# Kernel tuning notes

Measured on AMD Instinct MI355X. Metric: run time of the kernel, lower is better.

## Reference

```python
import jax, jax.numpy as jnp
import numpy as np

N_LAYERS = 2
N_QUBITS = 2


def _ry(t):
    c, s = jnp.cos(t / 2), jnp.sin(t / 2)
    m = jnp.stack([jnp.stack([c, -s], -1), jnp.stack([s, c], -1)], -2)
    return m.astype(jnp.complex64)


def _rx(t):
    c = jnp.cos(t / 2).astype(jnp.complex64)
    s = (-1j) * jnp.sin(t / 2).astype(jnp.complex64)
    return jnp.stack([jnp.stack([c, s], -1), jnp.stack([s, c], -1)], -2)


def _rz(t):
    e = jnp.exp(-0.5j * t.astype(jnp.complex64))
    z = jnp.zeros_like(e)
    return jnp.stack([jnp.stack([e, z], -1), jnp.stack([z, jnp.conj(e)], -1)], -2)


def _apply_w0(G, s):
    # gate on wire 0 (most significant); s: [N,2,2] indexed [n, q0, q1]
    if G.ndim == 2:
        G = G[None]
    return jnp.matmul(G, s)


def _apply_w1(G, s):
    # gate on wire 1: contract last index with G
    if G.ndim == 2:
        G = G[None]
    return jnp.matmul(s, jnp.swapaxes(G, -1, -2))


def _qnn_batched(enc, qw):
    # enc: [N,2] float angles; qw: [2,2,3] trainable angles.
    # Batched 2-qubit statevector simulation, state shape [N,2,2] (q0,q1).
    N = enc.shape[0]
    s = jnp.zeros((N, 2, 2), jnp.complex64).at[:, 0, 0].set(1.0)
    # data encoding: RY(enc_i) on wire i
    s = _apply_w0(_ry(enc[:, 0]), s)
    s = _apply_w1(_ry(enc[:, 1]), s)
    for l in range(N_LAYERS):
        # RX then RY then RZ on each qubit => fused single-qubit gate RZ@RY@RX
        g0 = _rz(qw[l, 0, 2]) @ _ry(qw[l, 0, 1]) @ _rx(qw[l, 0, 0])
        g1 = _rz(qw[l, 1, 2]) @ _ry(qw[l, 1, 1]) @ _rx(qw[l, 1, 0])
        s = _apply_w0(g0, s)
        s = _apply_w1(g1, s)
        # CNOT(control=0, target=1): flip q1 where q0 == 1
        s = s.at[:, 1, :].set(s[:, 1, ::-1])
    p = (s * jnp.conj(s)).real  # probabilities [N,2,2]
    z0 = (p[:, 0, :] - p[:, 1, :]).sum(-1)
    z1 = (p[:, :, 0] - p[:, :, 1]).sum(-1)
    return jnp.stack([z0, z1], -1)  # [N,2]


def _mlp(x, w1, b1, w2, b2, w3, b3):
    h = jnp.tanh(x @ w1 + b1)
    h = jnp.tanh(h @ w2 + b2)
    return h @ w3 + b3


def setup_inputs() -> dict:
    key = jax.random.key(0)
    ks = jax.random.split(key, 15)
    N = 1_000_000
    W = 32

    def rn(k, shape, scale):
        return (scale * jax.random.normal(k, shape)).astype(jnp.float32)

    return {
        "x": rn(ks[0], (N, 1), 1.0),
        "pre_w1": rn(ks[1], (1, W), 1.0),
        "pre_b1": rn(ks[2], (W,), 0.1),
        "pre_w2": rn(ks[3], (W, W), 1.0 / np.sqrt(W)),
        "pre_b2": rn(ks[4], (W,), 0.1),
        "pre_w3": rn(ks[5], (W, 2), 1.0 / np.sqrt(W)),
        "pre_b3": rn(ks[6], (2,), 0.1),
        "q_weights": rn(ks[7], (N_LAYERS, N_QUBITS, 3), 0.1),
        "post_w1": rn(ks[8], (2, W), 1.0 / np.sqrt(2)),
        "post_b1": rn(ks[9], (W,), 0.1),
        "post_w2": rn(ks[10], (W, W), 1.0 / np.sqrt(W)),
        "post_b2": rn(ks[11], (W,), 0.1),
        "post_w3": rn(ks[12], (W, 1), 1.0 / np.sqrt(W)),
        "post_b3": rn(ks[13], (1,), 0.1),
    }


def reference(x, pre_w1, pre_b1, pre_w2, pre_b2, pre_w3, pre_b3, q_weights,
              post_w1, post_b1, post_w2, post_b2, post_w3, post_b3):
    q = _mlp(x, pre_w1, pre_b1, pre_w2, pre_b2, pre_w3, pre_b3)        # [N,2]
    qhat = _qnn_batched(q, q_weights)                                  # [N,2]
    u = _mlp(qhat, post_w1, post_b1, post_w2, post_b2, post_w3, post_b3)  # [N,1]
    return u
```

## Files before the change

### kernel.cpp

```cpp
#include <hip/hip_runtime.h>
#include <math.h>
#include <stdint.h>


typedef __attribute__((ext_vector_type(8))) short short8;
typedef __attribute__((ext_vector_type(4))) float f32x4;

union Frag { uint32_t u[4]; short8 s; };

__device__ __forceinline__ float fast_tanh(float x) {
    float e = __expf(2.0f * x);
    return fmaf(-2.0f, __builtin_amdgcn_rcpf(e + 1.0f), 1.0f);
}

__device__ __forceinline__ void split8(const float h[8], uint32_t hi[4], uint32_t lo[4]) {
    #pragma unroll
    for (int p = 0; p < 4; ++p) {
        uint32_t u0 = __float_as_uint(h[2*p])   & 0xFFFF0000u;
        uint32_t u1 = __float_as_uint(h[2*p+1]) & 0xFFFF0000u;
        float l0 = h[2*p]   - __uint_as_float(u0);
        float l1 = h[2*p+1] - __uint_as_float(u1);
        uint32_t v0 = __float_as_uint(l0) & 0xFFFF0000u;
        uint32_t v1 = __float_as_uint(l1) & 0xFFFF0000u;
        hi[p] = (u0 >> 16) | u1;
        lo[p] = (v0 >> 16) | v1;
    }
}

struct cplx { float re, im; };
__device__ __forceinline__ cplx cmul(cplx a, cplx b) {
    return { a.re * b.re - a.im * b.im, a.re * b.im + a.im * b.re };
}
__device__ __forceinline__ cplx cadd(cplx a, cplx b) {
    return { a.re + b.re, a.im + b.im };
}

__global__ void qcpinn_setup(const float* __restrict__ qw,
                             const float* __restrict__ pw2,
                             const float* __restrict__ ow2,
                             float* __restrict__ ws) {
    const int lane = threadIdx.x & 63;
    const int s = lane & 15, gg = lane >> 4;
    uint32_t* wsu = (uint32_t*)ws;

    #pragma unroll
    for (int m = 0; m < 2; ++m) {
        const float* W = m ? ow2 : pw2;
        #pragma unroll
        for (int r = 0; r < 2; ++r) {
            float v[8];
            #pragma unroll
            for (int j = 0; j < 8; ++j)
                v[j] = W[(gg * 8 + j) * 32 + (r * 16 + s)];
            uint32_t hi[4], lo[4];
            split8(v, hi, lo);
            int bh = 32 + ((m * 4 + r * 2 + 0) * 64 + lane) * 4;
            int bl = 32 + ((m * 4 + r * 2 + 1) * 64 + lane) * 4;
            #pragma unroll
            for (int p = 0; p < 4; ++p) { wsu[bh + p] = hi[p]; wsu[bl + p] = lo[p]; }
        }
    }

    if (threadIdx.x == 0) {
        cplx U[16];
        for (int i = 0; i < 16; ++i) U[i] = {0.f, 0.f};
        U[0].re = U[5].re = U[10].re = U[15].re = 1.f;

        for (int l = 0; l < 2; ++l) {
            cplx g[2][4];
            for (int w = 0; w < 2; ++w) {
                float a = qw[l * 6 + w * 3 + 0];
                float b = qw[l * 6 + w * 3 + 1];
                float c = qw[l * 6 + w * 3 + 2];
                float sa, ca, sb, cb, sc, cc;
                __sincosf(0.5f * a, &sa, &ca);
                __sincosf(0.5f * b, &sb, &cb);
                __sincosf(0.5f * c, &sc, &cc);
                cplx RX[4] = {{ca, 0.f}, {0.f, -sa}, {0.f, -sa}, {ca, 0.f}};
                cplx RY[4] = {{cb, 0.f}, {-sb, 0.f}, {sb, 0.f}, {cb, 0.f}};
                cplx RZ[4] = {{cc, -sc}, {0.f, 0.f}, {0.f, 0.f}, {cc, sc}};
                cplx T[4];
                for (int i2 = 0; i2 < 2; ++i2)
                    for (int j2 = 0; j2 < 2; ++j2) {
                        cplx acc = {0.f, 0.f};
                        for (int k2 = 0; k2 < 2; ++k2)
                            acc = cadd(acc, cmul(RY[i2 * 2 + k2], RX[k2 * 2 + j2]));
                        T[i2 * 2 + j2] = acc;
                    }
                for (int i2 = 0; i2 < 2; ++i2)
                    for (int j2 = 0; j2 < 2; ++j2) {
                        cplx acc = {0.f, 0.f};
                        for (int k2 = 0; k2 < 2; ++k2)
                            acc = cadd(acc, cmul(RZ[i2 * 2 + k2], T[k2 * 2 + j2]));
                        g[w][i2 * 2 + j2] = acc;
                    }
            }
            cplx L[16];
            for (int i4 = 0; i4 < 4; ++i4) {
                int si = (i4 == 2) ? 3 : (i4 == 3) ? 2 : i4;
                for (int j4 = 0; j4 < 4; ++j4)
                    L[i4 * 4 + j4] = cmul(g[1][(si & 1) * 2 + (j4 & 1)],
                                          g[0][(si >> 1) * 2 + (j4 >> 1)]);
            }
            cplx Un[16];
            for (int i4 = 0; i4 < 4; ++i4)
                for (int j4 = 0; j4 < 4; ++j4) {
                    cplx acc = {0.f, 0.f};
                    for (int k4 = 0; k4 < 4; ++k4)
                        acc = cadd(acc, cmul(L[i4 * 4 + k4], U[k4 * 4 + j4]));
                    Un[i4 * 4 + j4] = acc;
                }
            for (int i = 0; i < 16; ++i) U[i] = Un[i];
        }
        for (int i = 0; i < 16; ++i) { ws[i] = U[i].re; ws[16 + i] = U[i].im; }
    }
}

__global__ __launch_bounds__(128) void qcpinn_main(
    const float* __restrict__ x,
    const float* __restrict__ pw1, const float* __restrict__ pb1,
    const float* __restrict__ pb2, const float* __restrict__ pw3,
    const float* __restrict__ pb3,
    const float* __restrict__ ws,
    const float* __restrict__ ow1, const float* __restrict__ ob1,
    const float* __restrict__ ob2, const float* __restrict__ ow3,
    const float* __restrict__ ob3,
    float* __restrict__ out, int N)
{
    const int lane = threadIdx.x & 63;
    const int wid  = threadIdx.x >> 6;
    const int s    = lane & 15;
    const int g    = lane >> 4;
    const int wave_id = blockIdx.x * 2 + wid;

    int samp[2];
    samp[0] = wave_id * 32 + s;
    samp[1] = samp[0] + 16;

    const float* U = ws;
    const Frag* fragp = (const Frag*)(ws + 32);

    float xv[2];
    xv[0] = (samp[0] < N) ? x[samp[0]] : 0.f;
    xv[1] = (samp[1] < N) ? x[samp[1]] : 0.f;

    f32x4 w1a = *(const f32x4*)(pw1 + g * 8);
    f32x4 w1b = *(const f32x4*)(pw1 + g * 8 + 4);
    f32x4 b1a = *(const f32x4*)(pb1 + g * 8);
    f32x4 b1b = *(const f32x4*)(pb1 + g * 8 + 4);

    Frag Bh[2], Bl[2];
    #pragma unroll
    for (int t = 0; t < 2; ++t) {
        float h[8];
        #pragma unroll
        for (int j = 0; j < 4; ++j) {
            h[j]     = fast_tanh(fmaf(xv[t], w1a[j], b1a[j]));
            h[4 + j] = fast_tanh(fmaf(xv[t], w1b[j], b1b[j]));
        }
        split8(h, Bh[t].u, Bl[t].u);
    }

    Frag A0h = fragp[0 * 64 + lane];
    Frag A0l = fragp[1 * 64 + lane];
    Frag A1h = fragp[2 * 64 + lane];
    Frag A1l = fragp[3 * 64 + lane];

    f32x4 pb2a = *(const f32x4*)(pb2 + g * 4);
    f32x4 pb2b = *(const f32x4*)(pb2 + 16 + g * 4);

    float h2[2][8];
    #pragma unroll
    for (int t = 0; t < 2; ++t) {
        f32x4 C0 = {0.f, 0.f, 0.f, 0.f};
        f32x4 C1 = {0.f, 0.f, 0.f, 0.f};
        C0 = __builtin_amdgcn_mfma_f32_16x16x32_bf16(A0h.s, Bh[t].s, C0, 0, 0, 0);
        C0 = __builtin_amdgcn_mfma_f32_16x16x32_bf16(A0h.s, Bl[t].s, C0, 0, 0, 0);
        C0 = __builtin_amdgcn_mfma_f32_16x16x32_bf16(A0l.s, Bh[t].s, C0, 0, 0, 0);
        C1 = __builtin_amdgcn_mfma_f32_16x16x32_bf16(A1h.s, Bh[t].s, C1, 0, 0, 0);
        C1 = __builtin_amdgcn_mfma_f32_16x16x32_bf16(A1h.s, Bl[t].s, C1, 0, 0, 0);
        C1 = __builtin_amdgcn_mfma_f32_16x16x32_bf16(A1l.s, Bh[t].s, C1, 0, 0, 0);
        #pragma unroll
        for (int i = 0; i < 4; ++i) {
            h2[t][i]     = fast_tanh(C0[i] + pb2a[i]);
            h2[t][4 + i] = fast_tanh(C1[i] + pb2b[i]);
        }
    }

    f32x4 w3a = *(const f32x4*)(pw3 + g * 8);
    f32x4 w3b = *(const f32x4*)(pw3 + g * 8 + 4);
    f32x4 w3c = *(const f32x4*)(pw3 + 32 + g * 8);
    f32x4 w3d = *(const f32x4*)(pw3 + 32 + g * 8 + 4);
    float bq0 = pb3[0], bq1 = pb3[1];

    float z0[2], z1[2];
    #pragma unroll
    for (int t = 0; t < 2; ++t) {
        float q0 = 0.f, q1 = 0.f;
        q0 = fmaf(h2[t][0], w3a[0], q0); q1 = fmaf(h2[t][0], w3a[1], q1);
        q0 = fmaf(h2[t][1], w3a[2], q0); q1 = fmaf(h2[t][1], w3a[3], q1);
        q0 = fmaf(h2[t][2], w3b[0], q0); q1 = fmaf(h2[t][2], w3b[1], q1);
        q0 = fmaf(h2[t][3], w3b[2], q0); q1 = fmaf(h2[t][3], w3b[3], q1);
        q0 = fmaf(h2[t][4], w3c[0], q0); q1 = fmaf(h2[t][4], w3c[1], q1);
        q0 = fmaf(h2[t][5], w3c[2], q0); q1 = fmaf(h2[t][5], w3c[3], q1);
        q0 = fmaf(h2[t][6], w3d[0], q0); q1 = fmaf(h2[t][6], w3d[1], q1);
        q0 = fmaf(h2[t][7], w3d[2], q0); q1 = fmaf(h2[t][7], w3d[3], q1);
        q0 += __shfl_xor(q0, 16); q0 += __shfl_xor(q0, 32);
        q1 += __shfl_xor(q1, 16); q1 += __shfl_xor(q1, 32);
        q0 += bq0; q1 += bq1;

        float s0, c0, s1, c1;
        __sincosf(0.5f * q0, &s0, &c0);
        __sincosf(0.5f * q1, &s1, &c1);
        float e0 = c0 * c1, e1 = c0 * s1, e2 = s0 * c1, e3 = s0 * s1;
        float p[4];
        #pragma unroll
        for (int m = 0; m < 4; ++m) {
            float re = fmaf(U[m * 4 + 0], e0, fmaf(U[m * 4 + 1], e1,
                       fmaf(U[m * 4 + 2], e2, U[m * 4 + 3] * e3)));
            float im = fmaf(U[16 + m * 4 + 0], e0, fmaf(U[16 + m * 4 + 1], e1,
                       fmaf(U[16 + m * 4 + 2], e2, U[16 + m * 4 + 3] * e3)));
            p[m] = fmaf(re, re, im * im);
        }
        z0[t] = p[0] + p[1] - p[2] - p[3];
        z1[t] = p[0] - p[1] + p[2] - p[3];
    }

    f32x4 oa  = *(const f32x4*)(ow1 + g * 8);
    f32x4 oa2 = *(const f32x4*)(ow1 + g * 8 + 4);
    f32x4 ob  = *(const f32x4*)(ow1 + 32 + g * 8);
    f32x4 ob2v= *(const f32x4*)(ow1 + 32 + g * 8 + 4);
    f32x4 obb = *(const f32x4*)(ob1 + g * 8);
    f32x4 obb2= *(const f32x4*)(ob1 + g * 8 + 4);

    Frag B2h[2], B2l[2];
    #pragma unroll
    for (int t = 0; t < 2; ++t) {
        float h[8];
        #pragma unroll
        for (int j = 0; j < 4; ++j) {
            h[j]     = fast_tanh(fmaf(z0[t], oa[j],  fmaf(z1[t], ob[j],   obb[j])));
            h[4 + j] = fast_tanh(fmaf(z0[t], oa2[j], fmaf(z1[t], ob2v[j], obb2[j])));
        }
        split8(h, B2h[t].u, B2l[t].u);
    }

    Frag P0h = fragp[4 * 64 + lane];
    Frag P0l = fragp[5 * 64 + lane];
    Frag P1h = fragp[6 * 64 + lane];
    Frag P1l = fragp[7 * 64 + lane];

    f32x4 ob2a = *(const f32x4*)(ob2 + g * 4);
    f32x4 ob2b = *(const f32x4*)(ob2 + 16 + g * 4);

    f32x4 w3o0 = *(const f32x4*)(ow3 + g * 4);
    f32x4 w3o1 = *(const f32x4*)(ow3 + 16 + g * 4);
    float bo = ob3[0];

    #pragma unroll
    for (int t = 0; t < 2; ++t) {
        f32x4 C0 = {0.f, 0.f, 0.f, 0.f};
        f32x4 C1 = {0.f, 0.f, 0.f, 0.f};
        C0 = __builtin_amdgcn_mfma_f32_16x16x32_bf16(P0h.s, B2h[t].s, C0, 0, 0, 0);
        C0 = __builtin_amdgcn_mfma_f32_16x16x32_bf16(P0h.s, B2l[t].s, C0, 0, 0, 0);
        C0 = __builtin_amdgcn_mfma_f32_16x16x32_bf16(P0l.s, B2h[t].s, C0, 0, 0, 0);
        C1 = __builtin_amdgcn_mfma_f32_16x16x32_bf16(P1h.s, B2h[t].s, C1, 0, 0, 0);
        C1 = __builtin_amdgcn_mfma_f32_16x16x32_bf16(P1h.s, B2l[t].s, C1, 0, 0, 0);
        C1 = __builtin_amdgcn_mfma_f32_16x16x32_bf16(P1l.s, B2h[t].s, C1, 0, 0, 0);

        float u = 0.f;
        #pragma unroll
        for (int i = 0; i < 4; ++i) {
            float ha = fast_tanh(C0[i] + ob2a[i]);
            float hb = fast_tanh(C1[i] + ob2b[i]);
            u = fmaf(ha, w3o0[i], u);
            u = fmaf(hb, w3o1[i], u);
        }
        u += __shfl_xor(u, 16);
        u += __shfl_xor(u, 32);
        u += bo;
        if (g == 0 && samp[t] < N) out[samp[t]] = u;
    }
}

extern "C" void kernel_launch(void* const* d_in, const int* in_sizes, int n_in,
                              void* d_out, int out_size, void* d_ws, size_t ws_size,
                              hipStream_t stream) {
    const float* x   = (const float*)d_in[0];
    const float* pw1 = (const float*)d_in[1];
    const float* pb1 = (const float*)d_in[2];
    const float* pw2 = (const float*)d_in[3];
    const float* pb2 = (const float*)d_in[4];
    const float* pw3 = (const float*)d_in[5];
    const float* pb3 = (const float*)d_in[6];
    const float* qw  = (const float*)d_in[7];
    const float* ow1 = (const float*)d_in[8];
    const float* ob1 = (const float*)d_in[9];
    const float* ow2 = (const float*)d_in[10];
    const float* ob2 = (const float*)d_in[11];
    const float* ow3 = (const float*)d_in[12];
    const float* ob3 = (const float*)d_in[13];
    float* out = (float*)d_out;
    float* ws  = (float*)d_ws;

    const int N = in_sizes[0];

    qcpinn_setup<<<1, 64, 0, stream>>>(qw, pw2, ow2, ws);

    const int grid = (N + 63) / 64;
    qcpinn_main<<<grid, 128, 0, stream>>>(
        x, pw1, pb1, pb2, pw3, pb3, ws,
        ow1, ob1, ob2, ow3, ob3, out, N);
}
```

Baseline: 130.3 us.

## Split quantum amplitude work across lane groups and process more samples per wave

Each 16-lane group now computes one of the four output amplitudes of the 2-qubit unitary, and the expectation values are combined with cross-lane shuffles. Before, every lane computed all four amplitudes redundantly. Each wave now handles 64 samples instead of 32, using blocks of 256 threads with a minimum-occupancy launch bound, which amortizes weight and fragment loads over more samples. tanh now calls the hardware exp2 builtin with a prescaled argument. The trade-off is extra shuffles and higher register pressure per wave.

```diff
diff --git a/kernel.cpp b/kernel.cpp
--- a/kernel.cpp
+++ b/kernel.cpp
@@ -9,7 +9,7 @@
 union Frag { uint32_t u[4]; short8 s; };
 
 __device__ __forceinline__ float fast_tanh(float x) {
-    float e = __expf(2.0f * x);
+    float e = __builtin_amdgcn_exp2f(x * 2.8853900817779268f);
     return fmaf(-2.0f, __builtin_amdgcn_rcpf(e + 1.0f), 1.0f);
 }
 
@@ -116,7 +116,8 @@
     }
 }
 
-__global__ __launch_bounds__(128) void qcpinn_main(
+#define NT 4
+__global__ __launch_bounds__(256, 4) void qcpinn_main(
     const float* __restrict__ x,
     const float* __restrict__ pw1, const float* __restrict__ pb1,
     const float* __restrict__ pb2, const float* __restrict__ pw3,
@@ -131,142 +132,125 @@
     const int wid  = threadIdx.x >> 6;
     const int s    = lane & 15;
     const int g    = lane >> 4;
-    const int wave_id = blockIdx.x * 2 + wid;
-
-    int samp[2];
-    samp[0] = wave_id * 32 + s;
-    samp[1] = samp[0] + 16;
-
-    const float* U = ws;
+    const int base = (blockIdx.x * 4 + wid) * (NT * 16);
+
     const Frag* fragp = (const Frag*)(ws + 32);
 
-    float xv[2];
-    xv[0] = (samp[0] < N) ? x[samp[0]] : 0.f;
-    xv[1] = (samp[1] < N) ? x[samp[1]] : 0.f;
+    float xv[NT];
+    #pragma unroll
+    for (int t = 0; t < NT; ++t) {
+        int idx = base + t * 16 + s;
+        xv[t] = (idx < N) ? x[idx] : 0.f;
+    }
 
     f32x4 w1a = *(const f32x4*)(pw1 + g * 8);
     f32x4 w1b = *(const f32x4*)(pw1 + g * 8 + 4);
     f32x4 b1a = *(const f32x4*)(pb1 + g * 8);
     f32x4 b1b = *(const f32x4*)(pb1 + g * 8 + 4);
-
-    Frag Bh[2], Bl[2];
-    #pragma unroll
-    for (int t = 0; t < 2; ++t) {
-        float h[8];
-        #pragma unroll
-        for (int j = 0; j < 4; ++j) {
-            h[j]     = fast_tanh(fmaf(xv[t], w1a[j], b1a[j]));
-            h[4 + j] = fast_tanh(fmaf(xv[t], w1b[j], b1b[j]));
-        }
-        split8(h, Bh[t].u, Bl[t].u);
-    }
-
     Frag A0h = fragp[0 * 64 + lane];
     Frag A0l = fragp[1 * 64 + lane];
     Frag A1h = fragp[2 * 64 + lane];
     Frag A1l = fragp[3 * 64 + lane];
-
     f32x4 pb2a = *(const f32x4*)(pb2 + g * 4);
     f32x4 pb2b = *(const f32x4*)(pb2 + 16 + g * 4);
-
-    float h2[2][8];
-    #pragma unroll
-    for (int t = 0; t < 2; ++t) {
-        f32x4 C0 = {0.f, 0.f, 0.f, 0.f};
-        f32x4 C1 = {0.f, 0.f, 0.f, 0.f};
-        C0 = __builtin_amdgcn_mfma_f32_16x16x32_bf16(A0h.s, Bh[t].s, C0, 0, 0, 0);
-        C0 = __builtin_amdgcn_mfma_f32_16x16x32_bf16(A0h.s, Bl[t].s, C0, 0, 0, 0);
-        C0 = __builtin_amdgcn_mfma_f32_16x16x32_bf16(A0l.s, Bh[t].s, C0, 0, 0, 0);
-        C1 = __builtin_amdgcn_mfma_f32_16x16x32_bf16(A1h.s, Bh[t].s, C1, 0, 0, 0);
-        C1 = __builtin_amdgcn_mfma_f32_16x16x32_bf16(A1h.s, Bl[t].s, C1, 0, 0, 0);
-        C1 = __builtin_amdgcn_mfma_f32_16x16x32_bf16(A1l.s, Bh[t].s, C1, 0, 0, 0);
-        #pragma unroll
-        for (int i = 0; i < 4; ++i) {
-            h2[t][i]     = fast_tanh(C0[i] + pb2a[i]);
-            h2[t][4 + i] = fast_tanh(C1[i] + pb2b[i]);
-        }
-    }
-
     f32x4 w3a = *(const f32x4*)(pw3 + g * 8);
     f32x4 w3b = *(const f32x4*)(pw3 + g * 8 + 4);
     f32x4 w3c = *(const f32x4*)(pw3 + 32 + g * 8);
     f32x4 w3d = *(const f32x4*)(pw3 + 32 + g * 8 + 4);
-    float bq0 = pb3[0], bq1 = pb3[1];
-
-    float z0[2], z1[2];
-    #pragma unroll
-    for (int t = 0; t < 2; ++t) {
+    const float bq0 = pb3[0], bq1 = pb3[1];
+    f32x4 Ure = *(const f32x4*)(ws + g * 4);
+    f32x4 Uim = *(const f32x4*)(ws + 16 + g * 4);
+    const float sgn0 = (g & 2) ? -1.f : 1.f;
+    const float sgn1 = (g & 1) ? -1.f : 1.f;
+
+    float z0[NT], z1[NT];
+    #pragma unroll
+    for (int t = 0; t < NT; ++t) {
+        float h[8];
+        #pragma unroll
+        for (int j = 0; j < 4; ++j) {
+            h[j]     = fast_tanh(fmaf(xv[t], w1a[j], b1a[j]));
+            h[4 + j] = fast_tanh(fmaf(xv[t], w1b[j], b1b[j]));
+        }
+        Frag Bh, Bl;
+        split8(h, Bh.u, Bl.u);
+
+        f32x4 C0 = {0.f, 0.f, 0.f, 0.f};
+        f32x4 C1 = {0.f, 0.f, 0.f, 0.f};
+        C0 = __builtin_amdgcn_mfma_f32_16x16x32_bf16(A0h.s, Bh.s, C0, 0, 0, 0);
+        C0 = __builtin_amdgcn_mfma_f32_16x16x32_bf16(A0h.s, Bl.s, C0, 0, 0, 0);
+        C0 = __builtin_amdgcn_mfma_f32_16x16x32_bf16(A0l.s, Bh.s, C0, 0, 0, 0);
+        C1 = __builtin_amdgcn_mfma_f32_16x16x32_bf16(A1h.s, Bh.s, C1, 0, 0, 0);
+        C1 = __builtin_amdgcn_mfma_f32_16x16x32_bf16(A1h.s, Bl.s, C1, 0, 0, 0);
+        C1 = __builtin_amdgcn_mfma_f32_16x16x32_bf16(A1l.s, Bh.s, C1, 0, 0, 0);
+
+        float h2[8];
+        #pragma unroll
+        for (int i = 0; i < 4; ++i) {
+            h2[i]     = fast_tanh(C0[i] + pb2a[i]);
+            h2[4 + i] = fast_tanh(C1[i] + pb2b[i]);
+        }
+
         float q0 = 0.f, q1 = 0.f;
-        q0 = fmaf(h2[t][0], w3a[0], q0); q1 = fmaf(h2[t][0], w3a[1], q1);
-        q0 = fmaf(h2[t][1], w3a[2], q0); q1 = fmaf(h2[t][1], w3a[3], q1);
-        q0 = fmaf(h2[t][2], w3b[0], q0); q1 = fmaf(h2[t][2], w3b[1], q1);
-        q0 = fmaf(h2[t][3], w3b[2], q0); q1 = fmaf(h2[t][3], w3b[3], q1);
-        q0 = fmaf(h2[t][4], w3c[0], q0); q1 = fmaf(h2[t][4], w3c[1], q1);
-        q0 = fmaf(h2[t][5], w3c[2], q0); q1 = fmaf(h2[t][5], w3c[3], q1);
-        q0 = fmaf(h2[t][6], w3d[0], q0); q1 = fmaf(h2[t][6], w3d[1], q1);
-        q0 = fmaf(h2[t][7], w3d[2], q0); q1 = fmaf(h2[t][7], w3d[3], q1);
-        q0 += __shfl_xor(q0, 16); q0 += __shfl_xor(q0, 32);
-        q1 += __shfl_xor(q1, 16); q1 += __shfl_xor(q1, 32);
-        q0 += bq0; q1 += bq1;
+        q0 = fmaf(h2[0], w3a[0], q0); q1 = fmaf(h2[0], w3a[1], q1);
+        q0 = fmaf(h2[1], w3a[2], q0); q1 = fmaf(h2[1], w3a[3], q1);
+        q0 = fmaf(h2[2], w3b[0], q0); q1 = fmaf(h2[2], w3b[1], q1);
+        q0 = fmaf(h2[3], w3b[2], q0); q1 = fmaf(h2[3], w3b[3], q1);
+        q0 = fmaf(h2[4], w3c[0], q0); q1 = fmaf(h2[4], w3c[1], q1);
+        q0 = fmaf(h2[5], w3c[2], q0); q1 = fmaf(h2[5], w3c[3], q1);
+        q0 = fmaf(h2[6], w3d[0], q0); q1 = fmaf(h2[6], w3d[1], q1);
+        q0 = fmaf(h2[7], w3d[2], q0); q1 = fmaf(h2[7], w3d[3], q1);
+        q0 += __shfl_xor(q0, 16); q0 += __shfl_xor(q0, 32); q0 += bq0;
+        q1 += __shfl_xor(q1, 16); q1 += __shfl_xor(q1, 32); q1 += bq1;
 
         float s0, c0, s1, c1;
         __sincosf(0.5f * q0, &s0, &c0);
         __sincosf(0.5f * q1, &s1, &c1);
         float e0 = c0 * c1, e1 = c0 * s1, e2 = s0 * c1, e3 = s0 * s1;
-        float p[4];
-        #pragma unroll
-        for (int m = 0; m < 4; ++m) {
-            float re = fmaf(U[m * 4 + 0], e0, fmaf(U[m * 4 + 1], e1,
-                       fmaf(U[m * 4 + 2], e2, U[m * 4 + 3] * e3)));
-            float im = fmaf(U[16 + m * 4 + 0], e0, fmaf(U[16 + m * 4 + 1], e1,
-                       fmaf(U[16 + m * 4 + 2], e2, U[16 + m * 4 + 3] * e3)));
-            p[m] = fmaf(re, re, im * im);
-        }
-        z0[t] = p[0] + p[1] - p[2] - p[3];
-        z1[t] = p[0] - p[1] + p[2] - p[3];
-    }
-
-    f32x4 oa  = *(const f32x4*)(ow1 + g * 8);
-    f32x4 oa2 = *(const f32x4*)(ow1 + g * 8 + 4);
-    f32x4 ob  = *(const f32x4*)(ow1 + 32 + g * 8);
-    f32x4 ob2v= *(const f32x4*)(ow1 + 32 + g * 8 + 4);
-    f32x4 obb = *(const f32x4*)(ob1 + g * 8);
-    f32x4 obb2= *(const f32x4*)(ob1 + g * 8 + 4);
-
-    Frag B2h[2], B2l[2];
-    #pragma unroll
-    for (int t = 0; t < 2; ++t) {
-        float h[8];
-        #pragma unroll
-        for (int j = 0; j < 4; ++j) {
-            h[j]     = fast_tanh(fmaf(z0[t], oa[j],  fmaf(z1[t], ob[j],   obb[j])));
-            h[4 + j] = fast_tanh(fmaf(z0[t], oa2[j], fmaf(z1[t], ob2v[j], obb2[j])));
-        }
-        split8(h, B2h[t].u, B2l[t].u);
-    }
-
+        float re = fmaf(Ure[0], e0, fmaf(Ure[1], e1, fmaf(Ure[2], e2, Ure[3] * e3)));
+        float im = fmaf(Uim[0], e0, fmaf(Uim[1], e1, fmaf(Uim[2], e2, Uim[3] * e3)));
+        float p  = fmaf(re, re, im * im);
+        float t0 = sgn0 * p, t1 = sgn1 * p;
+        t0 += __shfl_xor(t0, 16); t0 += __shfl_xor(t0, 32);
+        t1 += __shfl_xor(t1, 16); t1 += __shfl_xor(t1, 32);
+        z0[t] = t0; z1[t] = t1;
+    }
+
+    f32x4 oa   = *(const f32x4*)(ow1 + g * 8);
+    f32x4 oa2  = *(const f32x4*)(ow1 + g * 8 + 4);
+    f32x4 obv  = *(const f32x4*)(ow1 + 32 + g * 8);
+    f32x4 ob2v = *(const f32x4*)(ow1 + 32 + g * 8 + 4);
+    f32x4 obb  = *(const f32x4*)(ob1 + g * 8);
+    f32x4 obb2 = *(const f32x4*)(ob1 + g * 8 + 4);
     Frag P0h = fragp[4 * 64 + lane];
     Frag P0l = fragp[5 * 64 + lane];
     Frag P1h = fragp[6 * 64 + lane];
     Frag P1l = fragp[7 * 64 + lane];
-
     f32x4 ob2a = *(const f32x4*)(ob2 + g * 4);
     f32x4 ob2b = *(const f32x4*)(ob2 + 16 + g * 4);
-
     f32x4 w3o0 = *(const f32x4*)(ow3 + g * 4);
     f32x4 w3o1 = *(const f32x4*)(ow3 + 16 + g * 4);
-    float bo = ob3[0];
-
-    #pragma unroll
-    for (int t = 0; t < 2; ++t) {
+    const float bo = ob3[0];
+
+    #pragma unroll
+    for (int t = 0; t < NT; ++t) {
+        float h[8];
+        #pragma unroll
+        for (int j = 0; j < 4; ++j) {
+            h[j]     = fast_tanh(fmaf(z0[t], oa[j],  fmaf(z1[t], obv[j],  obb[j])));
+            h[4 + j] = fast_tanh(fmaf(z0[t], oa2[j], fmaf(z1[t], ob2v[j], obb2[j])));
+        }
+        Frag Bh, Bl;
+        split8(h, Bh.u, Bl.u);
+
         f32x4 C0 = {0.f, 0.f, 0.f, 0.f};
         f32x4 C1 = {0.f, 0.f, 0.f, 0.f};
-        C0 = __builtin_amdgcn_mfma_f32_16x16x32_bf16(P0h.s, B2h[t].s, C0, 0, 0, 0);
-        C0 = __builtin_amdgcn_mfma_f32_16x16x32_bf16(P0h.s, B2l[t].s, C0, 0, 0, 0);
-        C0 = __builtin_amdgcn_mfma_f32_16x16x32_bf16(P0l.s, B2h[t].s, C0, 0, 0, 0);
-        C1 = __builtin_amdgcn_mfma_f32_16x16x32_bf16(P1h.s, B2h[t].s, C1, 0, 0, 0);
-        C1 = __builtin_amdgcn_mfma_f32_16x16x32_bf16(P1h.s, B2l[t].s, C1, 0, 0, 0);
-        C1 = __builtin_amdgcn_mfma_f32_16x16x32_bf16(P1l.s, B2h[t].s, C1, 0, 0, 0);
+        C0 = __builtin_amdgcn_mfma_f32_16x16x32_bf16(P0h.s, Bh.s, C0, 0, 0, 0);
+        C0 = __builtin_amdgcn_mfma_f32_16x16x32_bf16(P0h.s, Bl.s, C0, 0, 0, 0);
+        C0 = __builtin_amdgcn_mfma_f32_16x16x32_bf16(P0l.s, Bh.s, C0, 0, 0, 0);
+        C1 = __builtin_amdgcn_mfma_f32_16x16x32_bf16(P1h.s, Bh.s, C1, 0, 0, 0);
+        C1 = __builtin_amdgcn_mfma_f32_16x16x32_bf16(P1h.s, Bl.s, C1, 0, 0, 0);
+        C1 = __builtin_amdgcn_mfma_f32_16x16x32_bf16(P1l.s, Bh.s, C1, 0, 0, 0);
 
         float u = 0.f;
         #pragma unroll
@@ -279,7 +263,8 @@
         u += __shfl_xor(u, 16);
         u += __shfl_xor(u, 32);
         u += bo;
-        if (g == 0 && samp[t] < N) out[samp[t]] = u;
+        int idx = base + t * 16 + s;
+        if (g == 0 && idx < N) out[idx] = u;
     }
 }
 
@@ -307,8 +292,8 @@
 
     qcpinn_setup<<<1, 64, 0, stream>>>(qw, pw2, ow2, ws);
 
-    const int grid = (N + 63) / 64;
-    qcpinn_main<<<grid, 128, 0, stream>>>(
+    const int grid = (N + 255) / 256;
+    qcpinn_main<<<grid, 256, 0, stream>>>(
         x, pw1, pb1, pb2, pw3, pb3, ws,
         ow1, ob1, ob2, ow3, ob3, out, N);
 }
```

Result: faster. 126.3 us (-3.1%).
